# Kernel optimization log

Hardware: AMD Instinct MI355X
Metric: run time of the kernel (lower is better)

## Reference

```python
import jax, jax.numpy as jnp
import numpy as np

N, M, K = 4096, 256, 32
W_EPS = 1e-6


def _spd(key, n, k):
    # well-conditioned SPD precision matrices: A A^T / k + I
    a = jax.random.normal(key, (n, k, k), dtype=jnp.float32)
    return jnp.matmul(a, jnp.swapaxes(a, -1, -2)) / k + jnp.eye(k, dtype=jnp.float32)


def setup_inputs() -> dict:
    key = jax.random.key(0)
    k1, k2, k3, k4 = jax.random.split(key, 4)
    W = jax.random.uniform(k1, (N, M), dtype=jnp.float32)
    mu_s = jax.random.normal(k2, (N, K), dtype=jnp.float32)
    omega_child = _spd(k3, N, K)
    omega_parent = _spd(k4, M, K)
    return {"W": W, "mu_s": mu_s, "omega_child": omega_child, "omega_parent": omega_parent}


def reference(W, mu_s, omega_child, omega_parent):
    # mask out negligible memberships (original skips w < 1e-6)
    wT = W.T                                   # (M, N)
    mask = wT >= W_EPS
    w = jnp.where(mask, wT, 0.0)

    # v_i = inv(omega_child_i) @ mu_s_i  -> batched solve, (N, K)
    v = jnp.linalg.solve(omega_child, mu_s[..., None])[..., 0]

    # transported means: Omega_alpha @ v_i, (M, N, K)
    T = jnp.einsum('mkl,nl->mnk', omega_parent, v)

    Z = w.sum(-1)                              # (M,)
    Zs = jnp.maximum(Z, 1e-30)
    mu_bar = jnp.einsum('mn,mnk->mk', w, T) / Zs[:, None]
    diff = T - mu_bar[:, None, :]              # (M, N, K)
    var = jnp.einsum('mn,mnk->mk', w, diff * diff) / Zs[:, None]
    psi = var.sum(-1)                          # (M,)

    # clusters with fewer than 2 contributing agents get psi = 0
    count = mask.sum(-1)
    return jnp.where(count >= 2, psi, 0.0)
```

## Files before the change

### kernel.cpp

```cpp
#include <hip/hip_runtime.h>

constexpr int N_AG = 4096;
constexpr int M_CL = 256;
constexpr int KD   = 32;
constexpr float WEPS = 1e-6f;

constexpr int PART_STRIDE = 1088;
constexpr int PART_SZ = M_CL * 4 * PART_STRIDE;
constexpr int VT_OFF  = PART_SZ;

typedef __attribute__((ext_vector_type(8))) short short8;
typedef __attribute__((ext_vector_type(4))) float f32x4;

__device__ __forceinline__ float rlane(float x, int l) {
    return __int_as_float(__builtin_amdgcn_readlane(__float_as_int(x), l));
}

__device__ __forceinline__ float fast_rcp(float x) {
#if __has_builtin(__builtin_amdgcn_rcpf)
    float r = __builtin_amdgcn_rcpf(x);
    return r * (2.0f - x * r);
#else
    return 1.0f / x;
#endif
}

template<int J>
struct FE {
    static __device__ __forceinline__ void run(float (&a)[32], float& rhs,
                                               float& pl, const int rr) {
        const float piv  = rlane(a[J], J);
        const float pinv = fast_rcp(piv);
        if (rr == J) pl = pinv;
        const float f = (rr > J) ? a[J] * pinv : 0.0f;
        #pragma unroll
        for (int j = J + 1; j < 32; ++j) {
            const float rJ = rlane(a[j], J);
            a[j] = fmaf(-f, rJ, a[j]);
        }
        const float rb = rlane(rhs, J);
        rhs = fmaf(-f, rb, rhs);
        FE<J + 1>::run(a, rhs, pl, rr);
    }
};
template<> struct FE<32> {
    static __device__ __forceinline__ void run(float (&)[32], float&, float&, const int) {}
};

template<int J>
struct BS {
    static __device__ __forceinline__ void run(const float (&a)[32], float& rhs,
                                               const float pl, float& xv, const int rr) {
        const float xj = rlane(rhs, J) * rlane(pl, J);
        if (rr == J) xv = xj;
        rhs = fmaf(-a[J], xj, rhs);
        BS<J - 1>::run(a, rhs, pl, xv, rr);
    }
};
template<> struct BS<-1> {
    static __device__ __forceinline__ void run(const float (&)[32], float&,
                                               const float, float&, const int) {}
};

__global__ __launch_bounds__(256) void solve_kernel(const float* __restrict__ mu,
                                                    const float* __restrict__ oc,
                                                    float* __restrict__ ws) {
    __shared__ float sv[4][32];
    const int t    = threadIdx.x;
    const int lane = t & 63;
    const int wid  = t >> 6;
    const int n0   = blockIdx.x * 4;
    const int idx  = n0 + wid;
    const int rr   = lane & 31;

    float a[32];
    const float4* src = reinterpret_cast<const float4*>(oc + (size_t)idx * 1024 + rr * 32);
    #pragma unroll
    for (int q = 0; q < 8; ++q) {
        const float4 t4 = src[q];
        a[4 * q + 0] = t4.x; a[4 * q + 1] = t4.y;
        a[4 * q + 2] = t4.z; a[4 * q + 3] = t4.w;
    }
    float rhs = mu[(size_t)idx * 32 + rr];
    float pl = 0.0f, xv = 0.0f;

    FE<0>::run(a, rhs, pl, rr);
    BS<31>::run(a, rhs, pl, xv, rr);

    if (lane < 32) sv[wid][lane] = xv;
    __syncthreads();
    if (t < 128) {
        const int k = t >> 2;
        const int j = t & 3;
        ws[VT_OFF + (size_t)k * 4096 + n0 + j] = sv[j][k];
    }
}

__global__ __launch_bounds__(256, 4) void partial_kernel(const float* __restrict__ W,
                                                         const float* __restrict__ vT,
                                                         float* __restrict__ wsout) {
    const int m = blockIdx.x >> 2;
    const int p = blockIdx.x & 3;
    const int t = threadIdx.x;
    const int lane = t & 63;
    const int wv   = t >> 6;

    __shared__ unsigned ubuf[4][2][32 * 36];
    __shared__ float swbuf[1024];
    float* const s1buf = swbuf;
    float* const zred  = swbuf + 32;

    const int rbase = p * 1024 + t * 4;
    const float w0 = W[(size_t)(rbase + 0) * 256 + m];
    const float w1 = W[(size_t)(rbase + 1) * 256 + m];
    const float w2 = W[(size_t)(rbase + 2) * 256 + m];
    const float w3 = W[(size_t)(rbase + 3) * 256 + m];
    const float m0 = (w0 >= WEPS) ? w0 : 0.0f;
    const float m1 = (w1 >= WEPS) ? w1 : 0.0f;
    const float m2 = (w2 >= WEPS) ? w2 : 0.0f;
    const float m3 = (w3 >= WEPS) ? w3 : 0.0f;
    float zacc = m0 + m1 + m2 + m3;
    float cacc = (w0 >= WEPS ? 1.f : 0.f) + (w1 >= WEPS ? 1.f : 0.f)
               + (w2 >= WEPS ? 1.f : 0.f) + (w3 >= WEPS ? 1.f : 0.f);
    reinterpret_cast<float4*>(swbuf)[t] =
        make_float4(sqrtf(m0), sqrtf(m1), sqrtf(m2), sqrtf(m3));

    f32x4 Chh[4], Chl[4];
    #pragma unroll
    for (int q = 0; q < 4; ++q) {
        Chh[q] = (f32x4){0.f, 0.f, 0.f, 0.f};
        Chl[q] = (f32x4){0.f, 0.f, 0.f, 0.f};
    }
    float s1acc[4] = {0.f, 0.f, 0.f, 0.f};

    const int krow = lane >> 3;
    const int nsub = (lane & 7) * 4;

    for (int rnd = 0; rnd < 4; ++rnd) {
        const int nloc0 = wv * 256 + rnd * 64;

        #pragma unroll
        for (int it = 0; it < 8; ++it) {
            const int k  = krow + 8 * (it & 3);
            const int nn = nsub + 32 * (it >> 2);
            const float4 v4 = *reinterpret_cast<const float4*>(
                vT + (size_t)k * 4096 + p * 1024 + nloc0 + nn);
            const float4 s4 = *reinterpret_cast<const float4*>(&swbuf[nloc0 + nn]);
            const float ux = v4.x * s4.x, uy = v4.y * s4.y;
            const float uz = v4.z * s4.z, uw = v4.w * s4.w;
            const unsigned bx = __float_as_uint(ux), by = __float_as_uint(uy);
            const unsigned bz = __float_as_uint(uz), bw = __float_as_uint(uw);
            const unsigned hi01 = __builtin_amdgcn_perm(by, bx, 0x07060302u);
            const unsigned hi23 = __builtin_amdgcn_perm(bw, bz, 0x07060302u);
            const float lx = ux - __uint_as_float(bx & 0xFFFF0000u);
            const float ly = uy - __uint_as_float(by & 0xFFFF0000u);
            const float lz = uz - __uint_as_float(bz & 0xFFFF0000u);
            const float lw = uw - __uint_as_float(bw & 0xFFFF0000u);
            const unsigned lo01 = __builtin_amdgcn_perm(__float_as_uint(ly), __float_as_uint(lx), 0x07060302u);
            const unsigned lo23 = __builtin_amdgcn_perm(__float_as_uint(lw), __float_as_uint(lz), 0x07060302u);
            const int dwi = k * 36 + (nn >> 1);
            *reinterpret_cast<uint2*>(&ubuf[wv][0][dwi]) = make_uint2(hi01, hi23);
            *reinterpret_cast<uint2*>(&ubuf[wv][1][dwi]) = make_uint2(lo01, lo23);
            s1acc[it & 3] += ux * s4.x + uy * s4.y + uz * s4.z + uw * s4.w;
        }

        #pragma unroll
        for (int c2 = 0; c2 < 2; ++c2) {
            const int ndw = (c2 * 32 + (lane >> 4) * 8) >> 1;
            const int r0 = (lane & 15) * 36 + ndw;
            const int r1 = r0 + 16 * 36;
            const short8 h0 = *reinterpret_cast<const short8*>(&ubuf[wv][0][r0]);
            const short8 h1 = *reinterpret_cast<const short8*>(&ubuf[wv][0][r1]);
            const short8 l0 = *reinterpret_cast<const short8*>(&ubuf[wv][1][r0]);
            const short8 l1 = *reinterpret_cast<const short8*>(&ubuf[wv][1][r1]);
            Chh[0] = __builtin_amdgcn_mfma_f32_16x16x32_bf16(h0, h0, Chh[0], 0, 0, 0);
            Chh[1] = __builtin_amdgcn_mfma_f32_16x16x32_bf16(h0, h1, Chh[1], 0, 0, 0);
            Chh[2] = __builtin_amdgcn_mfma_f32_16x16x32_bf16(h1, h0, Chh[2], 0, 0, 0);
            Chh[3] = __builtin_amdgcn_mfma_f32_16x16x32_bf16(h1, h1, Chh[3], 0, 0, 0);
            Chl[0] = __builtin_amdgcn_mfma_f32_16x16x32_bf16(h0, l0, Chl[0], 0, 0, 0);
            Chl[1] = __builtin_amdgcn_mfma_f32_16x16x32_bf16(h0, l1, Chl[1], 0, 0, 0);
            Chl[2] = __builtin_amdgcn_mfma_f32_16x16x32_bf16(h1, l0, Chl[2], 0, 0, 0);
            Chl[3] = __builtin_amdgcn_mfma_f32_16x16x32_bf16(h1, l1, Chl[3], 0, 0, 0);
        }
    }

    float* redw = reinterpret_cast<float*>(&ubuf[wv][0][0]);
    #pragma unroll
    for (int q = 0; q < 4; ++q) {
        #pragma unroll
        for (int r = 0; r < 4; ++r) {
            redw[q * 256 + r * 64 + lane] = Chh[q][r] + 2.0f * Chl[q][r];
        }
    }

    #pragma unroll
    for (int s = 1; s < 64; s <<= 1) {
        zacc += __shfl_xor(zacc, s);
        cacc += __shfl_xor(cacc, s);
    }

    __syncthreads();
    if (t < 32) s1buf[t] = 0.0f;
    if (lane == 0) { zred[wv] = zacc; zred[4 + wv] = cacc; }
    __syncthreads();

    #pragma unroll
    for (int j = 0; j < 4; ++j) {
        float r = s1acc[j];
        r += __shfl_xor(r, 1);
        r += __shfl_xor(r, 2);
        r += __shfl_xor(r, 4);
        if ((lane & 7) == 0) atomicAdd(&s1buf[krow + 8 * j], r);
    }
    __syncthreads();

    const size_t base = (size_t)(m * 4 + p) * PART_STRIDE;
    float o0 = 0.f, o1 = 0.f, o2 = 0.f, o3 = 0.f;
    #pragma unroll
    for (int ww = 0; ww < 4; ++ww) {
        const float4 x = *reinterpret_cast<const float4*>(
            &reinterpret_cast<float*>(&ubuf[ww][0][0])[t * 4]);
        o0 += x.x; o1 += x.y; o2 += x.z; o3 += x.w;
    }
    *reinterpret_cast<float4*>(&wsout[base + t * 4]) = make_float4(o0, o1, o2, o3);
    if (t == 0) wsout[base + 1056] = zred[0] + zred[1] + zred[2] + zred[3];
    if (t == 1) wsout[base + 1057] = zred[4] + zred[5] + zred[6] + zred[7];
    if (t < 32) wsout[base + 1024 + t] = s1buf[t];
}

__global__ __launch_bounds__(256) void combine_kernel(const float* __restrict__ op,
                                                      const float* __restrict__ ws,
                                                      float* __restrict__ out) {
    const int m = blockIdx.x;
    const int t = threadIdx.x;

    __shared__ float omg[32 * 33];
    __shared__ float vbar[32];
    __shared__ float red[256];

    #pragma unroll
    for (int i = 0; i < 4; ++i) {
        const int g = t + 256 * i;
        omg[(g >> 5) * 33 + (g & 31)] = op[(size_t)m * 1024 + g];
    }

    const int k  = t >> 3;
    const int l0 = (t & 7) * 4;
    const int pbase = ((k >> 4) * 2 + (l0 >> 4)) * 256
                    + (k & 3) * 64 + ((k >> 2) & 3) * 16 + (l0 & 15);

    const size_t mb = (size_t)m * 4 * PART_STRIDE;
    float Z = 0.0f, cnt = 0.0f, s1 = 0.0f;
    float s2[4] = {0.f, 0.f, 0.f, 0.f};
    #pragma unroll
    for (int p2 = 0; p2 < 4; ++p2) {
        const size_t bp = mb + (size_t)p2 * PART_STRIDE;
        Z   += ws[bp + 1056];
        cnt += ws[bp + 1057];
        if (t < 32) s1 += ws[bp + 1024 + t];
        const float4 sp = *reinterpret_cast<const float4*>(&ws[bp + pbase]);
        s2[0] += sp.x; s2[1] += sp.y; s2[2] += sp.z; s2[3] += sp.w;
    }
    const float invZ = 1.0f / fmaxf(Z, 1e-30f);
    if (t < 32) vbar[t] = s1 * invZ;
    __syncthreads();

    float G[4] = {0.f, 0.f, 0.f, 0.f};
    #pragma unroll
    for (int i = 0; i < 32; ++i) {
        const float ok = omg[i * 33 + k];
        #pragma unroll
        for (int q = 0; q < 4; ++q) G[q] = fmaf(ok, omg[i * 33 + l0 + q], G[q]);
    }

    const float vk = vbar[k];
    float val = 0.0f;
    #pragma unroll
    for (int q = 0; q < 4; ++q)
        val += G[q] * (s2[q] * invZ - vk * vbar[l0 + q]);

    red[t] = val; __syncthreads();
    #pragma unroll
    for (int s = 128; s > 0; s >>= 1) {
        if (t < s) red[t] += red[t + s];
        __syncthreads();
    }
    if (t == 0) out[m] = (cnt >= 1.5f) ? red[0] : 0.0f;
}

extern "C" void kernel_launch(void* const* d_in, const int* in_sizes, int n_in,
                              void* d_out, int out_size, void* d_ws, size_t ws_size,
                              hipStream_t stream) {
    const float* W  = (const float*)d_in[0];
    const float* mu = (const float*)d_in[1];
    const float* oc = (const float*)d_in[2];
    const float* op = (const float*)d_in[3];
    float* out = (float*)d_out;
    float* ws  = (float*)d_ws;

    solve_kernel<<<1024, 256, 0, stream>>>(mu, oc, ws);
    partial_kernel<<<1024, 256, 0, stream>>>(W, ws + VT_OFF, ws);
    combine_kernel<<<256, 256, 0, stream>>>(op, ws, out);
}
```

Measured before the change: 103.8 us.

## Fuse partial and combine kernels into one 1024-thread block per cluster

```diff
diff --git a/kernel.cpp b/kernel.cpp
--- a/kernel.cpp
+++ b/kernel.cpp
@@ -5,9 +5,7 @@
 constexpr int KD   = 32;
 constexpr float WEPS = 1e-6f;
 
-constexpr int PART_STRIDE = 1088;
-constexpr int PART_SZ = M_CL * 4 * PART_STRIDE;
-constexpr int VT_OFF  = PART_SZ;
+constexpr int VT_OFF = 0;
 
 typedef __attribute__((ext_vector_type(8))) short short8;
 typedef __attribute__((ext_vector_type(4))) float f32x4;
@@ -96,21 +94,25 @@
     }
 }
 
-__global__ __launch_bounds__(256, 4) void partial_kernel(const float* __restrict__ W,
-                                                         const float* __restrict__ vT,
-                                                         float* __restrict__ wsout) {
-    const int m = blockIdx.x >> 2;
-    const int p = blockIdx.x & 3;
-    const int t = threadIdx.x;
+__global__ __launch_bounds__(1024, 4) void fused_kernel(const float* __restrict__ W,
+                                                        const float* __restrict__ vT,
+                                                        const float* __restrict__ op,
+                                                        float* __restrict__ out) {
+    const int m  = blockIdx.x;
+    const int t  = threadIdx.x;
     const int lane = t & 63;
     const int wv   = t >> 6;
 
-    __shared__ unsigned ubuf[4][2][32 * 36];
-    __shared__ float swbuf[1024];
+    __shared__ unsigned ubuf[16][2][640];
+    __shared__ float swbuf[4096];
     float* const s1buf = swbuf;
-    float* const zred  = swbuf + 32;
-
-    const int rbase = p * 1024 + t * 4;
+    float* const zredL = swbuf + 32;
+    float* const credL = swbuf + 48;
+    float* const omg   = swbuf + 64;
+    float* const vbar  = swbuf + 1120;
+    float* const red2  = swbuf + 1152;
+
+    const int rbase = t * 4;
     const float w0 = W[(size_t)(rbase + 0) * 256 + m];
     const float w1 = W[(size_t)(rbase + 1) * 256 + m];
     const float w2 = W[(size_t)(rbase + 2) * 256 + m];
@@ -136,16 +138,15 @@
     const int krow = lane >> 3;
     const int nsub = (lane & 7) * 4;
 
-    for (int rnd = 0; rnd < 4; ++rnd) {
-        const int nloc0 = wv * 256 + rnd * 64;
-
-        #pragma unroll
-        for (int it = 0; it < 8; ++it) {
-            const int k  = krow + 8 * (it & 3);
-            const int nn = nsub + 32 * (it >> 2);
+    for (int rnd = 0; rnd < 8; ++rnd) {
+        const int nloc0 = wv * 256 + rnd * 32;
+
+        #pragma unroll
+        for (int it = 0; it < 4; ++it) {
+            const int k = krow + 8 * it;
             const float4 v4 = *reinterpret_cast<const float4*>(
-                vT + (size_t)k * 4096 + p * 1024 + nloc0 + nn);
-            const float4 s4 = *reinterpret_cast<const float4*>(&swbuf[nloc0 + nn]);
+                vT + (size_t)k * 4096 + nloc0 + nsub);
+            const float4 s4 = *reinterpret_cast<const float4*>(&swbuf[nloc0 + nsub]);
             const float ux = v4.x * s4.x, uy = v4.y * s4.y;
             const float uz = v4.z * s4.z, uw = v4.w * s4.w;
             const unsigned bx = __float_as_uint(ux), by = __float_as_uint(uy);
@@ -158,30 +159,26 @@
             const float lw = uw - __uint_as_float(bw & 0xFFFF0000u);
             const unsigned lo01 = __builtin_amdgcn_perm(__float_as_uint(ly), __float_as_uint(lx), 0x07060302u);
             const unsigned lo23 = __builtin_amdgcn_perm(__float_as_uint(lw), __float_as_uint(lz), 0x07060302u);
-            const int dwi = k * 36 + (nn >> 1);
+            const int dwi = k * 20 + (nsub >> 1);
             *reinterpret_cast<uint2*>(&ubuf[wv][0][dwi]) = make_uint2(hi01, hi23);
             *reinterpret_cast<uint2*>(&ubuf[wv][1][dwi]) = make_uint2(lo01, lo23);
-            s1acc[it & 3] += ux * s4.x + uy * s4.y + uz * s4.z + uw * s4.w;
+            s1acc[it] += ux * s4.x + uy * s4.y + uz * s4.z + uw * s4.w;
         }
 
-        #pragma unroll
-        for (int c2 = 0; c2 < 2; ++c2) {
-            const int ndw = (c2 * 32 + (lane >> 4) * 8) >> 1;
-            const int r0 = (lane & 15) * 36 + ndw;
-            const int r1 = r0 + 16 * 36;
-            const short8 h0 = *reinterpret_cast<const short8*>(&ubuf[wv][0][r0]);
-            const short8 h1 = *reinterpret_cast<const short8*>(&ubuf[wv][0][r1]);
-            const short8 l0 = *reinterpret_cast<const short8*>(&ubuf[wv][1][r0]);
-            const short8 l1 = *reinterpret_cast<const short8*>(&ubuf[wv][1][r1]);
-            Chh[0] = __builtin_amdgcn_mfma_f32_16x16x32_bf16(h0, h0, Chh[0], 0, 0, 0);
-            Chh[1] = __builtin_amdgcn_mfma_f32_16x16x32_bf16(h0, h1, Chh[1], 0, 0, 0);
-            Chh[2] = __builtin_amdgcn_mfma_f32_16x16x32_bf16(h1, h0, Chh[2], 0, 0, 0);
-            Chh[3] = __builtin_amdgcn_mfma_f32_16x16x32_bf16(h1, h1, Chh[3], 0, 0, 0);
-            Chl[0] = __builtin_amdgcn_mfma_f32_16x16x32_bf16(h0, l0, Chl[0], 0, 0, 0);
-            Chl[1] = __builtin_amdgcn_mfma_f32_16x16x32_bf16(h0, l1, Chl[1], 0, 0, 0);
-            Chl[2] = __builtin_amdgcn_mfma_f32_16x16x32_bf16(h1, l0, Chl[2], 0, 0, 0);
-            Chl[3] = __builtin_amdgcn_mfma_f32_16x16x32_bf16(h1, l1, Chl[3], 0, 0, 0);
-        }
+        const int r0 = (lane & 15) * 20 + ((lane >> 4) << 2);
+        const int r1 = r0 + 320;
+        const short8 h0 = *reinterpret_cast<const short8*>(&ubuf[wv][0][r0]);
+        const short8 h1 = *reinterpret_cast<const short8*>(&ubuf[wv][0][r1]);
+        const short8 l0 = *reinterpret_cast<const short8*>(&ubuf[wv][1][r0]);
+        const short8 l1 = *reinterpret_cast<const short8*>(&ubuf[wv][1][r1]);
+        Chh[0] = __builtin_amdgcn_mfma_f32_16x16x32_bf16(h0, h0, Chh[0], 0, 0, 0);
+        Chh[1] = __builtin_amdgcn_mfma_f32_16x16x32_bf16(h0, h1, Chh[1], 0, 0, 0);
+        Chh[2] = __builtin_amdgcn_mfma_f32_16x16x32_bf16(h1, h0, Chh[2], 0, 0, 0);
+        Chh[3] = __builtin_amdgcn_mfma_f32_16x16x32_bf16(h1, h1, Chh[3], 0, 0, 0);
+        Chl[0] = __builtin_amdgcn_mfma_f32_16x16x32_bf16(h0, l0, Chl[0], 0, 0, 0);
+        Chl[1] = __builtin_amdgcn_mfma_f32_16x16x32_bf16(h0, l1, Chl[1], 0, 0, 0);
+        Chl[2] = __builtin_amdgcn_mfma_f32_16x16x32_bf16(h1, l0, Chl[2], 0, 0, 0);
+        Chl[3] = __builtin_amdgcn_mfma_f32_16x16x32_bf16(h1, l1, Chl[3], 0, 0, 0);
     }
 
     float* redw = reinterpret_cast<float*>(&ubuf[wv][0][0]);
@@ -200,8 +197,16 @@
     }
 
     __syncthreads();
+
     if (t < 32) s1buf[t] = 0.0f;
-    if (lane == 0) { zred[wv] = zacc; zred[4 + wv] = cacc; }
+    if (lane == 0) { zredL[wv] = zacc; credL[wv] = cacc; }
+    omg[(t >> 5) * 33 + (t & 31)] = op[(size_t)m * 1024 + t];
+
+    float Ptot = 0.0f;
+    const float* ub = reinterpret_cast<const float*>(&ubuf[0][0][0]);
+    #pragma unroll
+    for (int ww = 0; ww < 16; ++ww) Ptot += ub[ww * 1280 + t];
+
     __syncthreads();
 
     #pragma unroll
@@ -214,78 +219,33 @@
     }
     __syncthreads();
 
-    const size_t base = (size_t)(m * 4 + p) * PART_STRIDE;
-    float o0 = 0.f, o1 = 0.f, o2 = 0.f, o3 = 0.f;
-    #pragma unroll
-    for (int ww = 0; ww < 4; ++ww) {
-        const float4 x = *reinterpret_cast<const float4*>(
-            &reinterpret_cast<float*>(&ubuf[ww][0][0])[t * 4]);
-        o0 += x.x; o1 += x.y; o2 += x.z; o3 += x.w;
-    }
-    *reinterpret_cast<float4*>(&wsout[base + t * 4]) = make_float4(o0, o1, o2, o3);
-    if (t == 0) wsout[base + 1056] = zred[0] + zred[1] + zred[2] + zred[3];
-    if (t == 1) wsout[base + 1057] = zred[4] + zred[5] + zred[6] + zred[7];
-    if (t < 32) wsout[base + 1024 + t] = s1buf[t];
-}
-
-__global__ __launch_bounds__(256) void combine_kernel(const float* __restrict__ op,
-                                                      const float* __restrict__ ws,
-                                                      float* __restrict__ out) {
-    const int m = blockIdx.x;
-    const int t = threadIdx.x;
-
-    __shared__ float omg[32 * 33];
-    __shared__ float vbar[32];
-    __shared__ float red[256];
-
-    #pragma unroll
-    for (int i = 0; i < 4; ++i) {
-        const int g = t + 256 * i;
-        omg[(g >> 5) * 33 + (g & 31)] = op[(size_t)m * 1024 + g];
-    }
-
-    const int k  = t >> 3;
-    const int l0 = (t & 7) * 4;
-    const int pbase = ((k >> 4) * 2 + (l0 >> 4)) * 256
-                    + (k & 3) * 64 + ((k >> 2) & 3) * 16 + (l0 & 15);
-
-    const size_t mb = (size_t)m * 4 * PART_STRIDE;
-    float Z = 0.0f, cnt = 0.0f, s1 = 0.0f;
-    float s2[4] = {0.f, 0.f, 0.f, 0.f};
-    #pragma unroll
-    for (int p2 = 0; p2 < 4; ++p2) {
-        const size_t bp = mb + (size_t)p2 * PART_STRIDE;
-        Z   += ws[bp + 1056];
-        cnt += ws[bp + 1057];
-        if (t < 32) s1 += ws[bp + 1024 + t];
-        const float4 sp = *reinterpret_cast<const float4*>(&ws[bp + pbase]);
-        s2[0] += sp.x; s2[1] += sp.y; s2[2] += sp.z; s2[3] += sp.w;
-    }
+    float Z = 0.0f, C = 0.0f;
+    #pragma unroll
+    for (int w = 0; w < 16; ++w) { Z += zredL[w]; C += credL[w]; }
     const float invZ = 1.0f / fmaxf(Z, 1e-30f);
-    if (t < 32) vbar[t] = s1 * invZ;
-    __syncthreads();
-
-    float G[4] = {0.f, 0.f, 0.f, 0.f};
-    #pragma unroll
-    for (int i = 0; i < 32; ++i) {
-        const float ok = omg[i * 33 + k];
-        #pragma unroll
-        for (int q = 0; q < 4; ++q) G[q] = fmaf(ok, omg[i * 33 + l0 + q], G[q]);
-    }
-
-    const float vk = vbar[k];
-    float val = 0.0f;
-    #pragma unroll
-    for (int q = 0; q < 4; ++q)
-        val += G[q] * (s2[q] * invZ - vk * vbar[l0 + q]);
-
-    red[t] = val; __syncthreads();
-    #pragma unroll
-    for (int s = 128; s > 0; s >>= 1) {
-        if (t < s) red[t] += red[t + s];
-        __syncthreads();
-    }
-    if (t == 0) out[m] = (cnt >= 1.5f) ? red[0] : 0.0f;
+    if (t < 32) vbar[t] = s1buf[t] * invZ;
+    __syncthreads();
+
+    const int q = t >> 8;
+    const int r = (t >> 6) & 3;
+    const int a = (q >> 1) * 16 + ((t >> 4) & 3) * 4 + r;
+    const int b = (q & 1) * 16 + (t & 15);
+    float G = 0.0f;
+    #pragma unroll
+    for (int i = 0; i < 32; ++i)
+        G = fmaf(omg[i * 33 + a], omg[i * 33 + b], G);
+    float val = G * (Ptot * invZ - vbar[a] * vbar[b]);
+
+    #pragma unroll
+    for (int s = 1; s < 64; s <<= 1) val += __shfl_xor(val, s);
+    if (lane == 0) red2[wv] = val;
+    __syncthreads();
+    if (t == 0) {
+        float acc = 0.0f;
+        #pragma unroll
+        for (int w = 0; w < 16; ++w) acc += red2[w];
+        out[m] = (C >= 1.5f) ? acc : 0.0f;
+    }
 }
 
 extern "C" void kernel_launch(void* const* d_in, const int* in_sizes, int n_in,
@@ -299,6 +259,5 @@
     float* ws  = (float*)d_ws;
 
     solve_kernel<<<1024, 256, 0, stream>>>(mu, oc, ws);
-    partial_kernel<<<1024, 256, 0, stream>>>(W, ws + VT_OFF, ws);
-    combine_kernel<<<256, 256, 0, stream>>>(op, ws, out);
-}
+    fused_kernel<<<256, 1024, 0, stream>>>(W, ws + VT_OFF, op, out);
+}
```

Measured after the change: 102.4 us, median of 2. No clear change (-1.4%).
